# Performance work log

Measured on AMD Instinct MI355X. Metric: run time of the kernel, lower is better.

## Reference

```python
import jax, jax.numpy as jnp
import numpy as np

N_EMBED = 1024
HEAD_COUNT = 16
HEAD_SIZE = 64  # HEAD_COUNT * HEAD_SIZE == N_EMBED
SEQ = 2048
BATCH = 2


def setup_inputs() -> dict:
    key = jax.random.key(0)
    k_ix, k_q, k_k, k_v, k_p, k_b = jax.random.split(key, 6)
    scale = 1.0 / np.sqrt(N_EMBED)
    inp = {
        "ix": jax.random.normal(k_ix, (BATCH, SEQ, N_EMBED), dtype=jnp.float32),
        # per-head projection weights, stored as x @ W form: [H, C, D]
        "Wq": jax.random.normal(k_q, (HEAD_COUNT, N_EMBED, HEAD_SIZE), dtype=jnp.float32) * scale,
        "Wk": jax.random.normal(k_k, (HEAD_COUNT, N_EMBED, HEAD_SIZE), dtype=jnp.float32) * scale,
        "Wv": jax.random.normal(k_v, (HEAD_COUNT, N_EMBED, HEAD_SIZE), dtype=jnp.float32) * scale,
        # output projection (Linear with bias): y = x @ Wp + bp
        "Wp": jax.random.normal(k_p, (N_EMBED, N_EMBED), dtype=jnp.float32) * scale,
        "bp": jax.random.normal(k_b, (N_EMBED,), dtype=jnp.float32) * scale,
    }
    return inp


def reference(ix, Wq, Wk, Wv, Wp, bp):
    B, T, C = ix.shape
    # per-head projections: [B, H, T, D]
    Q = jnp.einsum("btc,hcd->bhtd", ix, Wq)
    K = jnp.einsum("btc,hcd->bhtd", ix, Wk)
    V = jnp.einsum("btc,hcd->bhtd", ix, Wv)
    # NOTE: faithful to source -- scores are MULTIPLIED by sqrt(C) (C = n_embed)
    scores = jnp.einsum("bhtd,bhsd->bhts", Q, K) * (C ** 0.5)
    causal = jnp.tril(jnp.ones((T, T), dtype=bool))
    scores = jnp.where(causal, scores, -jnp.inf)
    wei = jax.nn.softmax(scores, axis=-1)
    out = jnp.einsum("bhts,bhsd->bhtd", wei, V)
    # concat heads (matches torch.cat over per-head outputs along last dim)
    out = out.transpose(0, 2, 1, 3).reshape(B, T, -1)
    return out @ Wp + bp
```

## Files before the change

kernel.cpp:

```cpp
#include <hip/hip_runtime.h>

#define BATCH 2
#define SEQL  2048
#define NEMB  1024
#define NH    16
#define HD    64
#define MROWS (BATCH*SEQL)

#define QSCALE 46.166241308446828f

typedef short bf16x8 __attribute__((ext_vector_type(8)));
typedef float f32x16 __attribute__((ext_vector_type(16)));

__device__ __forceinline__ unsigned short f2bf(float x) {
    union { float f; unsigned u; } v; v.f = x;
    unsigned r = v.u + 0x7FFFu + ((v.u >> 16) & 1u);
    return (unsigned short)(r >> 16);
}
__device__ __forceinline__ void split_bf16(float x, unsigned short& hi, unsigned short& lo) {
    hi = f2bf(x);
    union { unsigned u; float f; } h; h.u = ((unsigned)hi) << 16;
    lo = f2bf(x - h.f);
}
__device__ __forceinline__ unsigned cvt_pk_bf16(float a, float b) {
    unsigned r;
    asm("v_cvt_pk_bf16_f32 %0, %1, %2" : "=v"(r) : "v"(a), "v"(b));
    return r;
}
__device__ __forceinline__ void plane_swap(unsigned& a, unsigned& b) {
    asm volatile("v_permlane32_swap_b32 %0, %1" : "+v"(a), "+v"(b));
}

__device__ __forceinline__ int slot16(int chunk, int lane) {
    return chunk * 66 + (lane & 31) + 33 * (lane >> 5);
}

__global__ __launch_bounds__(256) void split_convert_kernel(
    const float* __restrict__ src,
    unsigned short* __restrict__ dhi, unsigned short* __restrict__ dlo)
{
    int i = (blockIdx.x * 256 + threadIdx.x) * 4;
    float4 v = *(const float4*)(src + i);
    unsigned short h[4], l[4];
    split_bf16(v.x, h[0], l[0]); split_bf16(v.y, h[1], l[1]);
    split_bf16(v.z, h[2], l[2]); split_bf16(v.w, h[3], l[3]);
    uint2 ph, pl;
    ph.x = h[0] | ((unsigned)h[1] << 16); ph.y = h[2] | ((unsigned)h[3] << 16);
    pl.x = l[0] | ((unsigned)l[1] << 16); pl.y = l[2] | ((unsigned)l[3] << 16);
    *(uint2*)(dhi + i) = ph;
    *(uint2*)(dlo + i) = pl;
}

__global__ __launch_bounds__(256) void transpose_convert_kernel(
    const float* __restrict__ Wq, const float* __restrict__ Wk,
    const float* __restrict__ Wv, const float* __restrict__ Wp,
    unsigned short* __restrict__ qhi, unsigned short* __restrict__ qlo,
    unsigned short* __restrict__ khi, unsigned short* __restrict__ klo,
    unsigned short* __restrict__ vhi, unsigned short* __restrict__ pt)
{
    __shared__ float tile[64][68];
    const int z = blockIdx.z, hb = blockIdx.y, c0 = blockIdx.x * 64;
    const float* src; int rstride; unsigned short* dhi; unsigned short* dlo;
    if (z == 0)      { src = Wq + (size_t)hb * 65536; rstride = 64;   dhi = qhi; dlo = qlo; }
    else if (z == 1) { src = Wk + (size_t)hb * 65536; rstride = 64;   dhi = khi; dlo = klo; }
    else if (z == 2) { src = Wv + (size_t)hb * 65536; rstride = 64;   dhi = vhi; dlo = nullptr; }
    else             { src = Wp + (size_t)hb * 64;    rstride = 1024; dhi = pt;  dlo = nullptr; }
    const int tid = threadIdx.x;
    #pragma unroll
    for (int i = 0; i < 4; ++i) {
        int fidx = i * 256 + tid;
        int r  = fidx >> 4;
        int dq = (fidx & 15) * 4;
        float4 v = *(const float4*)(src + (size_t)(c0 + r) * rstride + dq);
        *(float4*)&tile[r][dq] = v;
    }
    __syncthreads();
    #pragma unroll
    for (int i = 0; i < 4; ++i) {
        int fidx = i * 256 + tid;
        int d  = fidx >> 4;
        int cq = (fidx & 15) * 4;
        size_t base = (size_t)(hb * 64 + d) * 1024 + c0 + cq;
        unsigned short hh[4], ll[4];
        #pragma unroll
        for (int j = 0; j < 4; ++j) split_bf16(tile[cq + j][d], hh[j], ll[j]);
        uint2 ph; ph.x = hh[0] | ((unsigned)hh[1] << 16); ph.y = hh[2] | ((unsigned)hh[3] << 16);
        *(uint2*)(dhi + base) = ph;
        if (dlo) {
            uint2 pl; pl.x = ll[0] | ((unsigned)ll[1] << 16); pl.y = ll[2] | ((unsigned)ll[3] << 16);
            *(uint2*)(dlo + base) = pl;
        }
    }
}

__global__ __launch_bounds__(256, 2) void qkv_gemm(
    const unsigned short* __restrict__ Ahi, const unsigned short* __restrict__ Alo,
    const unsigned short* __restrict__ Bq_hi, const unsigned short* __restrict__ Bq_lo,
    const unsigned short* __restrict__ Bk_hi, const unsigned short* __restrict__ Bk_lo,
    const unsigned short* __restrict__ Bv_hi,
    unsigned short* __restrict__ Qhi, unsigned short* __restrict__ Qlo,
    unsigned short* __restrict__ Khi, unsigned short* __restrict__ Klo,
    unsigned short* __restrict__ Vt)
{
    __shared__ unsigned short smem[2][4][4224];

    const int z = blockIdx.z;
    const bool split = (z < 2);
    const unsigned short* __restrict__ Bhi = (z == 0) ? Bq_hi : (z == 1) ? Bk_hi : Bv_hi;
    const unsigned short* __restrict__ Blo = (z == 0) ? Bq_lo : Bk_lo;
    unsigned short* __restrict__ Ohi = (z == 0) ? Qhi : Khi;
    unsigned short* __restrict__ Olo = (z == 0) ? Qlo : Klo;
    const float oscale = (z == 0) ? QSCALE : 1.0f;

    const int m0 = blockIdx.x * 128;
    const int n0 = blockIdx.y * 128;
    const int tid  = threadIdx.x;
    const int wid  = tid >> 6, lane = tid & 63;
    const int wr   = wid >> 1, wc = wid & 1;

    int roff_[2], slot_[2];
    #pragma unroll
    for (int q = 0; q < 2; ++q) {
        int f   = q * 256 + tid;
        int row = f >> 2;
        int k8  = (f & 3) * 8;
        roff_[q] = row * 1024 + k8;
        slot_[q] = slot16((row >> 5) * 2 + (k8 >> 4), (row & 31) + 32 * ((k8 >> 3) & 1)) * 8;
    }
    const unsigned short* __restrict__ Ah = Ahi + (size_t)m0 * 1024;
    const unsigned short* __restrict__ Bh = Bhi + (size_t)n0 * 1024;
    const unsigned short* __restrict__ Al = split ? Alo + (size_t)m0 * 1024 : Ahi;
    const unsigned short* __restrict__ Bl = split ? Blo + (size_t)n0 * 1024 : Bhi;

    bf16x8 pah[2], pbh[2], pal[2], pbl[2];

    #define LOADT(KK)  do { _Pragma("unroll")                                   \
        for (int q = 0; q < 2; ++q) {                                           \
            pah[q] = *(const bf16x8*)(Ah + roff_[q] + (KK));                    \
            pbh[q] = *(const bf16x8*)(Bh + roff_[q] + (KK));                    \
            if (split) {                                                        \
                pal[q] = *(const bf16x8*)(Al + roff_[q] + (KK));                \
                pbl[q] = *(const bf16x8*)(Bl + roff_[q] + (KK));                \
            }                                                                   \
        } } while (0)

    #define WRITET(NB) do { _Pragma("unroll")                                   \
        for (int q = 0; q < 2; ++q) {                                           \
            *(bf16x8*)(&smem[NB][0][slot_[q]]) = pah[q];                        \
            *(bf16x8*)(&smem[NB][1][slot_[q]]) = pbh[q];                        \
            if (split) {                                                        \
                *(bf16x8*)(&smem[NB][2][slot_[q]]) = pal[q];                    \
                *(bf16x8*)(&smem[NB][3][slot_[q]]) = pbl[q];                    \
            }                                                                   \
        } } while (0)

    f32x16 acc[2][2] = {};

    LOADT(0);
    WRITET(0);
    LOADT(32);

    for (int t = 0; t < 32; ++t) {
        __syncthreads();
        if (t + 1 < 32) {
            WRITET((t + 1) & 1);
            if (t + 2 < 32) LOADT((t + 2) * 32);
        }
        const int cb = t & 1;
        const unsigned short* a_hi = smem[cb][0];
        const unsigned short* b_hi = smem[cb][1];
        const unsigned short* a_lo = smem[cb][2];
        const unsigned short* b_lo = smem[cb][3];

        #pragma unroll
        for (int kch = 0; kch < 2; ++kch) {
            bf16x8 ah[2], bh_[2];
            #pragma unroll
            for (int mt = 0; mt < 2; ++mt)
                ah[mt] = *(const bf16x8*)(a_hi + slot16((2 * wr + mt) * 2 + kch, lane) * 8);
            #pragma unroll
            for (int nt = 0; nt < 2; ++nt)
                bh_[nt] = *(const bf16x8*)(b_hi + slot16((2 * wc + nt) * 2 + kch, lane) * 8);
            if (split) {
                bf16x8 al[2], bl[2];
                #pragma unroll
                for (int mt = 0; mt < 2; ++mt)
                    al[mt] = *(const bf16x8*)(a_lo + slot16((2 * wr + mt) * 2 + kch, lane) * 8);
                #pragma unroll
                for (int nt = 0; nt < 2; ++nt)
                    bl[nt] = *(const bf16x8*)(b_lo + slot16((2 * wc + nt) * 2 + kch, lane) * 8);
                #pragma unroll
                for (int mt = 0; mt < 2; ++mt)
                    #pragma unroll
                    for (int nt = 0; nt < 2; ++nt) {
                        acc[mt][nt] = __builtin_amdgcn_mfma_f32_32x32x16_bf16(ah[mt], bh_[nt], acc[mt][nt], 0, 0, 0);
                        acc[mt][nt] = __builtin_amdgcn_mfma_f32_32x32x16_bf16(ah[mt], bl[nt],  acc[mt][nt], 0, 0, 0);
                        acc[mt][nt] = __builtin_amdgcn_mfma_f32_32x32x16_bf16(al[mt], bh_[nt], acc[mt][nt], 0, 0, 0);
                    }
            } else {
                #pragma unroll
                for (int mt = 0; mt < 2; ++mt)
                    #pragma unroll
                    for (int nt = 0; nt < 2; ++nt)
                        acc[mt][nt] = __builtin_amdgcn_mfma_f32_32x32x16_bf16(bh_[nt], ah[mt], acc[mt][nt], 0, 0, 0);
            }
        }
    }
    #undef LOADT
    #undef WRITET

    #pragma unroll
    for (int mt = 0; mt < 2; ++mt) {
        #pragma unroll
        for (int nt = 0; nt < 2; ++nt) {
            if (z == 2) {
                const int mcol = m0 + wr * 64 + mt * 32 + (lane & 31);
                const int bb = mcol >> 11, tt = mcol & (SEQL - 1);
                #pragma unroll
                for (int r = 0; r < 16; ++r) {
                    int nrow = n0 + wc * 64 + nt * 32 + (r & 3) + 8 * (r >> 2) + 4 * (lane >> 5);
                    int head = nrow >> 6, dd = nrow & 63;
                    Vt[((size_t)(bb * NH + head) * HD + dd) * SEQL + tt] = f2bf(acc[mt][nt][r]);
                }
            } else {
                const int ncol = n0 + wc * 64 + nt * 32 + (lane & 31);
                const int head = ncol >> 6, d = ncol & 63;
                #pragma unroll
                for (int r = 0; r < 16; ++r) {
                    int mrow = m0 + wr * 64 + mt * 32 + (r & 3) + 8 * (r >> 2) + 4 * (lane >> 5);
                    int bb = mrow >> 11, t = mrow & (SEQL - 1);
                    size_t idx = ((size_t)(bb * NH + head) * SEQL + t) * HD + d;
                    float v = acc[mt][nt][r] * oscale;
                    unsigned short hi = f2bf(v);
                    Ohi[idx] = hi;
                    union { unsigned u; float f; } hf; hf.u = ((unsigned)hi) << 16;
                    Olo[idx] = f2bf(v - hf.f);
                }
            }
        }
    }
}

__global__ __launch_bounds__(256) void attn_mfma_kernel(
    const unsigned short* __restrict__ Qhi, const unsigned short* __restrict__ Qlo,
    const unsigned short* __restrict__ Khi, const unsigned short* __restrict__ Klo,
    const unsigned short* __restrict__ Vt,
    unsigned short* __restrict__ AO)
{
    __shared__ unsigned short smem[2][3][4224];

    const int bid = blockIdx.x;
    const int xcd = bid & 7;
    const int idx = bid >> 3;
    const int bh  = xcd * 4 + (idx & 3);
    const int g   = idx >> 2;

    const int tid  = threadIdx.x;
    const int wid  = tid >> 6;
    const int lane = tid & 63;
    const int ln   = lane & 31;
    const int h    = lane >> 5;

    const int qb_idx = ((wid & 1) ? (31 - g) : g) + ((wid & 2) << 4);
    const int qb     = qb_idx * 32;
    const int qglob  = qb + ln;
    const int my_nt  = (qb_idx >> 1) + 1;
    const int tmax   = ((63 - g) >> 1) + 1;

    const unsigned short* __restrict__ Qbh = Qhi + (size_t)bh * SEQL * HD;
    const unsigned short* __restrict__ Qbl = Qlo + (size_t)bh * SEQL * HD;
    const unsigned short* __restrict__ Kbh = Khi + (size_t)bh * SEQL * HD;
    const unsigned short* __restrict__ Kbl = Klo + (size_t)bh * SEQL * HD;
    const unsigned short* __restrict__ Vtb = Vt  + (size_t)bh * HD * SEQL;

    bf16x8 qhi[4], qlo[4];
    #pragma unroll
    for (int c = 0; c < 4; ++c) {
        qhi[c] = *(const bf16x8*)(Qbh + (size_t)qglob * HD + c * 16 + h * 8);
        qlo[c] = *(const bf16x8*)(Qbl + (size_t)qglob * HD + c * 16 + h * 8);
    }

    int s_[2], d8_[2], ks_[2];
    #pragma unroll
    for (int ff = 0; ff < 2; ++ff) {
        int fidx = ff * 256 + tid;
        s_[ff]  = fidx >> 3;
        d8_[ff] = fidx & 7;
        ks_[ff] = slot16((s_[ff] >> 5) * 4 + (d8_[ff] >> 1),
                         (s_[ff] & 31) + 32 * (d8_[ff] & 1)) * 8;
    }

    bf16x8 kh[2], kl[2], vv[2];
    #pragma unroll
    for (int ff = 0; ff < 2; ++ff) {
        kh[ff] = *(const bf16x8*)(Kbh + (size_t)s_[ff] * HD + d8_[ff] * 8);
        kl[ff] = *(const bf16x8*)(Kbl + (size_t)s_[ff] * HD + d8_[ff] * 8);
        vv[ff] = *(const bf16x8*)(Vtb + (size_t)s_[ff] * SEQL + d8_[ff] * 8);
    }
    #pragma unroll
    for (int ff = 0; ff < 2; ++ff) {
        *(bf16x8*)(&smem[0][0][ks_[ff]]) = kh[ff];
        *(bf16x8*)(&smem[0][1][ks_[ff]]) = kl[ff];
        *(bf16x8*)(&smem[0][2][ks_[ff]]) = vv[ff];
    }
    if (tmax > 1) {
        #pragma unroll
        for (int ff = 0; ff < 2; ++ff) {
            kh[ff] = *(const bf16x8*)(Kbh + (size_t)(64 + s_[ff]) * HD + d8_[ff] * 8);
            kl[ff] = *(const bf16x8*)(Kbl + (size_t)(64 + s_[ff]) * HD + d8_[ff] * 8);
            vv[ff] = *(const bf16x8*)(Vtb + (size_t)s_[ff] * SEQL + 64 + d8_[ff] * 8);
        }
    }

    f32x16 oacc[2] = {};
    float m_run = -1e30f, l_run = 0.f;

    for (int t = 0; t < tmax; ++t) {
        __syncthreads();
        if (t + 1 < tmax) {
            const int nb = (t + 1) & 1;
            #pragma unroll
            for (int ff = 0; ff < 2; ++ff) {
                *(bf16x8*)(&smem[nb][0][ks_[ff]]) = kh[ff];
                *(bf16x8*)(&smem[nb][1][ks_[ff]]) = kl[ff];
                *(bf16x8*)(&smem[nb][2][ks_[ff]]) = vv[ff];
            }
            if (t + 2 < tmax) {
                const int s0n = (t + 2) * 64;
                #pragma unroll
                for (int ff = 0; ff < 2; ++ff) {
                    kh[ff] = *(const bf16x8*)(Kbh + (size_t)(s0n + s_[ff]) * HD + d8_[ff] * 8);
                    kl[ff] = *(const bf16x8*)(Kbl + (size_t)(s0n + s_[ff]) * HD + d8_[ff] * 8);
                    vv[ff] = *(const bf16x8*)(Vtb + (size_t)s_[ff] * SEQL + s0n + d8_[ff] * 8);
                }
            }
        }

        if (t < my_nt) {
            const int cb = t & 1;
            const int s0 = t * 64;
            const bf16x8* khf = (const bf16x8*)&smem[cb][0][0];
            const bf16x8* klf = (const bf16x8*)&smem[cb][1][0];
            const bf16x8* vtf = (const bf16x8*)&smem[cb][2][0];

            f32x16 sacc[2] = {};
            __builtin_amdgcn_s_setprio(1);
            #pragma unroll
            for (int sb = 0; sb < 2; ++sb) {
                #pragma unroll
                for (int c = 0; c < 4; ++c) {
                    bf16x8 ah = khf[slot16(sb * 4 + c, lane)];
                    bf16x8 al = klf[slot16(sb * 4 + c, lane)];
                    sacc[sb] = __builtin_amdgcn_mfma_f32_32x32x16_bf16(ah, qhi[c], sacc[sb], 0, 0, 0);
                    sacc[sb] = __builtin_amdgcn_mfma_f32_32x32x16_bf16(ah, qlo[c], sacc[sb], 0, 0, 0);
                    sacc[sb] = __builtin_amdgcn_mfma_f32_32x32x16_bf16(al, qhi[c], sacc[sb], 0, 0, 0);
                }
            }
            __builtin_amdgcn_s_setprio(0);

            if ((s0 + 63) > qb) {
                #pragma unroll
                for (int sb = 0; sb < 2; ++sb)
                    #pragma unroll
                    for (int r = 0; r < 16; ++r) {
                        int srow = (r & 3) + 8 * (r >> 2) + 4 * h + sb * 32;
                        if ((s0 + srow) > qglob) sacc[sb][r] = -1e30f;
                    }
            }

            float mtile = -1e30f;
            #pragma unroll
            for (int sb = 0; sb < 2; ++sb)
                #pragma unroll
                for (int r = 0; r < 16; ++r)
                    mtile = fmaxf(mtile, sacc[sb][r]);
            mtile = fmaxf(mtile, __shfl_xor(mtile, 32));

            if (!__all(mtile - m_run <= 11.5f)) {
                const float mnew  = fmaxf(m_run, mtile);
                const float alpha = exp2f(m_run - mnew);
                l_run *= alpha;
                #pragma unroll
                for (int dt = 0; dt < 2; ++dt)
                    #pragma unroll
                    for (int r = 0; r < 16; ++r)
                        oacc[dt][r] *= alpha;
                m_run = mnew;
            }

            float ps0 = 0.f, ps1 = 0.f;
            unsigned pw[2][8];
            #pragma unroll
            for (int sb = 0; sb < 2; ++sb) {
                #pragma unroll
                for (int r2 = 0; r2 < 8; ++r2) {
                    float p0 = exp2f(sacc[sb][2 * r2]     - m_run);
                    float p1 = exp2f(sacc[sb][2 * r2 + 1] - m_run);
                    if (sb == 0) ps0 += p0 + p1; else ps1 += p0 + p1;
                    pw[sb][r2] = cvt_pk_bf16(p0, p1);
                }
            }
            float psum = ps0 + ps1;
            psum += __shfl_xor(psum, 32);
            l_run += psum;

            bf16x8 pfrag[4];
            #pragma unroll
            for (int sb = 0; sb < 2; ++sb) {
                #pragma unroll
                for (int c = 0; c < 2; ++c) {
                    unsigned u0 = pw[sb][4 * c + 0], u2 = pw[sb][4 * c + 2];
                    unsigned u1 = pw[sb][4 * c + 1], u3 = pw[sb][4 * c + 3];
                    plane_swap(u0, u2);
                    plane_swap(u1, u3);
                    union { unsigned u[4]; bf16x8 v; } cvt;
                    cvt.u[0] = u0; cvt.u[1] = u1; cvt.u[2] = u2; cvt.u[3] = u3;
                    pfrag[sb * 2 + c] = cvt.v;
                }
            }

            __builtin_amdgcn_s_setprio(1);
            #pragma unroll
            for (int dt = 0; dt < 2; ++dt)
                #pragma unroll
                for (int sc = 0; sc < 4; ++sc)
                    oacc[dt] = __builtin_amdgcn_mfma_f32_32x32x16_bf16(
                        vtf[slot16(dt * 4 + sc, lane)], pfrag[sc], oacc[dt], 0, 0, 0);
            __builtin_amdgcn_s_setprio(0);
        }
    }

    const float inv = 1.0f / l_run;
    unsigned short* aop = AO + ((size_t)(bh >> 4) * SEQL + qglob) * NEMB + (bh & 15) * HD;
    #pragma unroll
    for (int dt = 0; dt < 2; ++dt) {
        #pragma unroll
        for (int rg = 0; rg < 4; ++rg) {
            int d0 = dt * 32 + rg * 8 + h * 4;
            uint2 w;
            w.x = cvt_pk_bf16(oacc[dt][rg * 4 + 0] * inv, oacc[dt][rg * 4 + 1] * inv);
            w.y = cvt_pk_bf16(oacc[dt][rg * 4 + 2] * inv, oacc[dt][rg * 4 + 3] * inv);
            *(uint2*)(aop + d0) = w;
        }
    }
}

__global__ __launch_bounds__(256, 2) void out_proj_kernel(
    const unsigned short* __restrict__ A, const unsigned short* __restrict__ B,
    const float* __restrict__ bias, float* __restrict__ out)
{
    __shared__ unsigned short smem[2][2][4224];

    const int m0 = blockIdx.x * 128;
    const int n0 = blockIdx.y * 128;
    const int tid  = threadIdx.x;
    const int wid  = tid >> 6, lane = tid & 63;
    const int wr   = wid >> 1, wc = wid & 1;

    int roff_[2], slot_[2];
    #pragma unroll
    for (int q = 0; q < 2; ++q) {
        int f   = q * 256 + tid;
        int row = f >> 2;
        int k8  = (f & 3) * 8;
        roff_[q] = row * 1024 + k8;
        slot_[q] = slot16((row >> 5) * 2 + (k8 >> 4), (row & 31) + 32 * ((k8 >> 3) & 1)) * 8;
    }
    const unsigned short* __restrict__ Ab = A + (size_t)m0 * 1024;
    const unsigned short* __restrict__ Bb = B + (size_t)n0 * 1024;

    bf16x8 pa[2], pb[2];
    #pragma unroll
    for (int q = 0; q < 2; ++q) {
        pa[q] = *(const bf16x8*)(Ab + roff_[q]);
        pb[q] = *(const bf16x8*)(Bb + roff_[q]);
    }
    #pragma unroll
    for (int q = 0; q < 2; ++q) {
        *(bf16x8*)(&smem[0][0][slot_[q]]) = pa[q];
        *(bf16x8*)(&smem[0][1][slot_[q]]) = pb[q];
    }
    #pragma unroll
    for (int q = 0; q < 2; ++q) {
        pa[q] = *(const bf16x8*)(Ab + roff_[q] + 32);
        pb[q] = *(const bf16x8*)(Bb + roff_[q] + 32);
    }

    f32x16 acc[2][2] = {};

    for (int t = 0; t < 32; ++t) {
        __syncthreads();
        if (t + 1 < 32) {
            const int nb = (t + 1) & 1;
            #pragma unroll
            for (int q = 0; q < 2; ++q) {
                *(bf16x8*)(&smem[nb][0][slot_[q]]) = pa[q];
                *(bf16x8*)(&smem[nb][1][slot_[q]]) = pb[q];
            }
            if (t + 2 < 32) {
                #pragma unroll
                for (int q = 0; q < 2; ++q) {
                    pa[q] = *(const bf16x8*)(Ab + roff_[q] + (t + 2) * 32);
                    pb[q] = *(const bf16x8*)(Bb + roff_[q] + (t + 2) * 32);
                }
            }
        }
        const int cb = t & 1;
        const unsigned short* a_s = smem[cb][0];
        const unsigned short* b_s = smem[cb][1];
        #pragma unroll
        for (int kch = 0; kch < 2; ++kch) {
            bf16x8 ah[2], bh_[2];
            #pragma unroll
            for (int mt = 0; mt < 2; ++mt)
                ah[mt] = *(const bf16x8*)(a_s + slot16((2 * wr + mt) * 2 + kch, lane) * 8);
            #pragma unroll
            for (int nt = 0; nt < 2; ++nt)
                bh_[nt] = *(const bf16x8*)(b_s + slot16((2 * wc + nt) * 2 + kch, lane) * 8);
            #pragma unroll
            for (int mt = 0; mt < 2; ++mt)
                #pragma unroll
                for (int nt = 0; nt < 2; ++nt)
                    acc[mt][nt] = __builtin_amdgcn_mfma_f32_32x32x16_bf16(ah[mt], bh_[nt], acc[mt][nt], 0, 0, 0);
        }
    }

    #pragma unroll
    for (int mt = 0; mt < 2; ++mt) {
        #pragma unroll
        for (int nt = 0; nt < 2; ++nt) {
            const int ncol = n0 + wc * 64 + nt * 32 + (lane & 31);
            const float bv = bias[ncol];
            #pragma unroll
            for (int r = 0; r < 16; ++r) {
                int mrow = m0 + wr * 64 + mt * 32 + (r & 3) + 8 * (r >> 2) + 4 * (lane >> 5);
                out[(size_t)mrow * 1024 + ncol] = acc[mt][nt][r] + bv;
            }
        }
    }
}

extern "C" void kernel_launch(void* const* d_in, const int* in_sizes, int n_in,
                              void* d_out, int out_size, void* d_ws, size_t ws_size,
                              hipStream_t stream)
{
    const float* ix = (const float*)d_in[0];
    const float* Wq = (const float*)d_in[1];
    const float* Wk = (const float*)d_in[2];
    const float* Wv = (const float*)d_in[3];
    const float* Wp = (const float*)d_in[4];
    const float* bp = (const float*)d_in[5];
    float* out = (float*)d_out;

    char* ws = (char*)d_ws;
    #define WSOFF(mb) ((unsigned short*)(ws + (size_t)(mb) * 1024 * 1024))
    unsigned short* ix_hi  = WSOFF(0);
    unsigned short* ix_lo  = WSOFF(8);
    unsigned short* Wqt_hi = WSOFF(16);
    unsigned short* Wqt_lo = WSOFF(18);
    unsigned short* Wkt_hi = WSOFF(20);
    unsigned short* Wkt_lo = WSOFF(22);
    unsigned short* Wvt_hi = WSOFF(24);
    unsigned short* Qhi    = WSOFF(26);
    unsigned short* Qlo    = WSOFF(34);
    unsigned short* Khi    = WSOFF(42);
    unsigned short* Klo    = WSOFF(50);
    unsigned short* Wpt    = WSOFF(58);
    unsigned short* AObf   = WSOFF(0);
    unsigned short* Vt     = (unsigned short*)d_out;
    #undef WSOFF

    split_convert_kernel<<<MROWS * NEMB / 4 / 256, 256, 0, stream>>>(ix, ix_hi, ix_lo);
    transpose_convert_kernel<<<dim3(16, 16, 4), 256, 0, stream>>>(
        Wq, Wk, Wv, Wp, Wqt_hi, Wqt_lo, Wkt_hi, Wkt_lo, Wvt_hi, Wpt);
    qkv_gemm<<<dim3(MROWS / 128, NEMB / 128, 3), 256, 0, stream>>>(
        ix_hi, ix_lo, Wqt_hi, Wqt_lo, Wkt_hi, Wkt_lo, Wvt_hi,
        Qhi, Qlo, Khi, Klo, Vt);
    attn_mfma_kernel<<<512, 256, 0, stream>>>(Qhi, Qlo, Khi, Klo, Vt, AObf);
    out_proj_kernel<<<dim3(MROWS / 128, NEMB / 128), 256, 0, stream>>>(AObf, Wpt, bp, out);
}
```

Before: 189.3 us.

## Split attention KV range across two blocks and merge partial softmax results

```diff
diff --git a/kernel.cpp b/kernel.cpp
--- a/kernel.cpp
+++ b/kernel.cpp
@@ -21,6 +21,10 @@
     hi = f2bf(x);
     union { unsigned u; float f; } h; h.u = ((unsigned)hi) << 16;
     lo = f2bf(x - h.f);
+}
+__device__ __forceinline__ float bf2f(unsigned short b) {
+    union { unsigned u; float f; } v; v.u = ((unsigned)b) << 16;
+    return v.f;
 }
 __device__ __forceinline__ unsigned cvt_pk_bf16(float a, float b) {
     unsigned r;
@@ -245,15 +249,18 @@
     const unsigned short* __restrict__ Qhi, const unsigned short* __restrict__ Qlo,
     const unsigned short* __restrict__ Khi, const unsigned short* __restrict__ Klo,
     const unsigned short* __restrict__ Vt,
-    unsigned short* __restrict__ AO)
+    unsigned short* __restrict__ Op0, unsigned short* __restrict__ Op1,
+    float* __restrict__ Ml)
 {
     __shared__ unsigned short smem[2][3][4224];
 
-    const int bid = blockIdx.x;
-    const int xcd = bid & 7;
-    const int idx = bid >> 3;
-    const int bh  = xcd * 4 + (idx & 3);
-    const int g   = idx >> 2;
+    const int bid  = blockIdx.x;
+    const int xcd  = bid & 7;
+    const int idx  = bid >> 3;
+    const int bh   = xcd * 4 + (idx & 3);
+    const int rest = idx >> 2;
+    const int j    = 15 - (rest >> 1);
+    const int sp   = rest & 1;
 
     const int tid  = threadIdx.x;
     const int wid  = tid >> 6;
@@ -261,11 +268,12 @@
     const int ln   = lane & 31;
     const int h    = lane >> 5;
 
-    const int qb_idx = ((wid & 1) ? (31 - g) : g) + ((wid & 2) << 4);
+    const int qb_idx = 4 * j + wid;
     const int qb     = qb_idx * 32;
     const int qglob  = qb + ln;
-    const int my_nt  = (qb_idx >> 1) + 1;
-    const int tmax   = ((63 - g) >> 1) + 1;
+    const int cutoff = 2 * j + (wid >> 1);
+    const int tbeg   = sp ? (j + 1) : 0;
+    const int tend   = sp ? (2 * j + 2) : (j + 1);
 
     const unsigned short* __restrict__ Qbh = Qhi + (size_t)bh * SEQL * HD;
     const unsigned short* __restrict__ Qbl = Qlo + (size_t)bh * SEQL * HD;
@@ -291,33 +299,38 @@
     }
 
     bf16x8 kh[2], kl[2], vv[2];
-    #pragma unroll
-    for (int ff = 0; ff < 2; ++ff) {
-        kh[ff] = *(const bf16x8*)(Kbh + (size_t)s_[ff] * HD + d8_[ff] * 8);
-        kl[ff] = *(const bf16x8*)(Kbl + (size_t)s_[ff] * HD + d8_[ff] * 8);
-        vv[ff] = *(const bf16x8*)(Vtb + (size_t)s_[ff] * SEQL + d8_[ff] * 8);
-    }
-    #pragma unroll
-    for (int ff = 0; ff < 2; ++ff) {
-        *(bf16x8*)(&smem[0][0][ks_[ff]]) = kh[ff];
-        *(bf16x8*)(&smem[0][1][ks_[ff]]) = kl[ff];
-        *(bf16x8*)(&smem[0][2][ks_[ff]]) = vv[ff];
-    }
-    if (tmax > 1) {
+    {
+        const int s0p = tbeg * 64;
         #pragma unroll
         for (int ff = 0; ff < 2; ++ff) {
-            kh[ff] = *(const bf16x8*)(Kbh + (size_t)(64 + s_[ff]) * HD + d8_[ff] * 8);
-            kl[ff] = *(const bf16x8*)(Kbl + (size_t)(64 + s_[ff]) * HD + d8_[ff] * 8);
-            vv[ff] = *(const bf16x8*)(Vtb + (size_t)s_[ff] * SEQL + 64 + d8_[ff] * 8);
+            kh[ff] = *(const bf16x8*)(Kbh + (size_t)(s0p + s_[ff]) * HD + d8_[ff] * 8);
+            kl[ff] = *(const bf16x8*)(Kbl + (size_t)(s0p + s_[ff]) * HD + d8_[ff] * 8);
+            vv[ff] = *(const bf16x8*)(Vtb + (size_t)s_[ff] * SEQL + s0p + d8_[ff] * 8);
+        }
+        const int pb = tbeg & 1;
+        #pragma unroll
+        for (int ff = 0; ff < 2; ++ff) {
+            *(bf16x8*)(&smem[pb][0][ks_[ff]]) = kh[ff];
+            *(bf16x8*)(&smem[pb][1][ks_[ff]]) = kl[ff];
+            *(bf16x8*)(&smem[pb][2][ks_[ff]]) = vv[ff];
+        }
+        if (tbeg + 1 < tend) {
+            const int s0n = (tbeg + 1) * 64;
+            #pragma unroll
+            for (int ff = 0; ff < 2; ++ff) {
+                kh[ff] = *(const bf16x8*)(Kbh + (size_t)(s0n + s_[ff]) * HD + d8_[ff] * 8);
+                kl[ff] = *(const bf16x8*)(Kbl + (size_t)(s0n + s_[ff]) * HD + d8_[ff] * 8);
+                vv[ff] = *(const bf16x8*)(Vtb + (size_t)s_[ff] * SEQL + s0n + d8_[ff] * 8);
+            }
         }
     }
 
     f32x16 oacc[2] = {};
     float m_run = -1e30f, l_run = 0.f;
 
-    for (int t = 0; t < tmax; ++t) {
+    for (int t = tbeg; t < tend; ++t) {
         __syncthreads();
-        if (t + 1 < tmax) {
+        if (t + 1 < tend) {
             const int nb = (t + 1) & 1;
             #pragma unroll
             for (int ff = 0; ff < 2; ++ff) {
@@ -325,7 +338,7 @@
                 *(bf16x8*)(&smem[nb][1][ks_[ff]]) = kl[ff];
                 *(bf16x8*)(&smem[nb][2][ks_[ff]]) = vv[ff];
             }
-            if (t + 2 < tmax) {
+            if (t + 2 < tend) {
                 const int s0n = (t + 2) * 64;
                 #pragma unroll
                 for (int ff = 0; ff < 2; ++ff) {
@@ -336,7 +349,7 @@
             }
         }
 
-        if (t < my_nt) {
+        if (t <= cutoff) {
             const int cb = t & 1;
             const int s0 = t * 64;
             const bf16x8* khf = (const bf16x8*)&smem[cb][0][0];
@@ -430,19 +443,57 @@
         }
     }
 
-    const float inv = 1.0f / l_run;
-    unsigned short* aop = AO + ((size_t)(bh >> 4) * SEQL + qglob) * NEMB + (bh & 15) * HD;
+    unsigned short* op = (sp ? Op1 : Op0)
+        + ((size_t)(bh >> 4) * SEQL + qglob) * NEMB + (bh & 15) * HD;
     #pragma unroll
     for (int dt = 0; dt < 2; ++dt) {
         #pragma unroll
         for (int rg = 0; rg < 4; ++rg) {
             int d0 = dt * 32 + rg * 8 + h * 4;
             uint2 w;
-            w.x = cvt_pk_bf16(oacc[dt][rg * 4 + 0] * inv, oacc[dt][rg * 4 + 1] * inv);
-            w.y = cvt_pk_bf16(oacc[dt][rg * 4 + 2] * inv, oacc[dt][rg * 4 + 3] * inv);
-            *(uint2*)(aop + d0) = w;
-        }
-    }
+            w.x = cvt_pk_bf16(oacc[dt][rg * 4 + 0], oacc[dt][rg * 4 + 1]);
+            w.y = cvt_pk_bf16(oacc[dt][rg * 4 + 2], oacc[dt][rg * 4 + 3]);
+            *(uint2*)(op + d0) = w;
+        }
+    }
+    if (h == 0) {
+        float2 mlv; mlv.x = m_run; mlv.y = l_run;
+        *(float2*)(Ml + ((size_t)(sp * 32 + bh) * SEQL + qglob) * 2) = mlv;
+    }
+}
+
+__global__ __launch_bounds__(256) void attn_merge_kernel(
+    unsigned short* __restrict__ Op0, const unsigned short* __restrict__ Op1,
+    const float* __restrict__ Ml)
+{
+    const int gid  = blockIdx.x * 256 + threadIdx.x;
+    const int row  = gid >> 7;
+    const int col  = (gid & 127) * 8;
+    const int bh   = ((row >> 11) << 4) + (col >> 6);
+    const int q    = row & (SEQL - 1);
+
+    float2 ml0 = *(const float2*)(Ml + ((size_t)bh * SEQL + q) * 2);
+    float2 ml1 = *(const float2*)(Ml + ((size_t)(32 + bh) * SEQL + q) * 2);
+    const float M  = fmaxf(ml0.x, ml1.x);
+    const float w0 = exp2f(ml0.x - M);
+    const float w1 = exp2f(ml1.x - M);
+    const float rd = 1.0f / (ml0.y * w0 + ml1.y * w1);
+    const float f0 = w0 * rd, f1 = w1 * rd;
+
+    size_t off = (size_t)row * NEMB + col;
+    uint4 a = *(const uint4*)(Op0 + off);
+    uint4 b = *(const uint4*)(Op1 + off);
+    const unsigned short* ap = (const unsigned short*)&a;
+    const unsigned short* bp = (const unsigned short*)&b;
+    uint4 o;
+    unsigned* opw = (unsigned*)&o;
+    #pragma unroll
+    for (int i = 0; i < 4; ++i) {
+        float r0 = bf2f(ap[2*i])     * f0 + bf2f(bp[2*i])     * f1;
+        float r1 = bf2f(ap[2*i + 1]) * f0 + bf2f(bp[2*i + 1]) * f1;
+        opw[i] = cvt_pk_bf16(r0, r1);
+    }
+    *(uint4*)(Op0 + off) = o;
 }
 
 __global__ __launch_bounds__(256, 2) void out_proj_kernel(
@@ -566,7 +617,9 @@
     unsigned short* Khi    = WSOFF(42);
     unsigned short* Klo    = WSOFF(50);
     unsigned short* Wpt    = WSOFF(58);
-    unsigned short* AObf   = WSOFF(0);
+    unsigned short* Op0    = WSOFF(0);
+    unsigned short* Op1    = WSOFF(8);
+    float*          Ml     = (float*)WSOFF(16);
     unsigned short* Vt     = (unsigned short*)d_out;
     #undef WSOFF
 
@@ -576,6 +629,7 @@
     qkv_gemm<<<dim3(MROWS / 128, NEMB / 128, 3), 256, 0, stream>>>(
         ix_hi, ix_lo, Wqt_hi, Wqt_lo, Wkt_hi, Wkt_lo, Wvt_hi,
         Qhi, Qlo, Khi, Klo, Vt);
-    attn_mfma_kernel<<<512, 256, 0, stream>>>(Qhi, Qlo, Khi, Klo, Vt, AObf);
-    out_proj_kernel<<<dim3(MROWS / 128, NEMB / 128), 256, 0, stream>>>(AObf, Wpt, bp, out);
-}
+    attn_mfma_kernel<<<1024, 256, 0, stream>>>(Qhi, Qlo, Khi, Klo, Vt, Op0, Op1, Ml);
+    attn_merge_kernel<<<MROWS * NEMB / 8 / 256, 256, 0, stream>>>(Op0, Op1, Ml);
+    out_proj_kernel<<<dim3(MROWS / 128, NEMB / 128), 256, 0, stream>>>(Op0, Wpt, bp, out);
+}
```

New measurement: 176.2 us. 1.07x faster.
